# Kernel tuning notes

Measured on AMD Instinct MI355X. Metric: run time of the kernel, lower is better.

## Reference

```python
import jax, jax.numpy as jnp
import numpy as np

D_MODEL = 1024
N_HEADS = 16
MAX_LAG = 512
D_K = D_MODEL // N_HEADS


def setup_inputs() -> dict:
    key = jax.random.key(0)
    ks = jax.random.split(key, 11)
    B, S = 2, 2048
    x = jax.random.normal(ks[0], (B, S, D_MODEL), dtype=jnp.float32)
    lag = jax.random.randint(ks[1], (S,), 0, MAX_LAG + 1, dtype=jnp.int64)
    scale = 1.0 / np.sqrt(D_MODEL)
    wq = jax.random.normal(ks[2], (D_MODEL, D_MODEL), dtype=jnp.float32) * scale
    bq = jnp.zeros((D_MODEL,), dtype=jnp.float32)
    wk = jax.random.normal(ks[3], (D_MODEL, D_MODEL), dtype=jnp.float32) * scale
    bk = jnp.zeros((D_MODEL,), dtype=jnp.float32)
    wv = jax.random.normal(ks[4], (D_MODEL, D_MODEL), dtype=jnp.float32) * scale
    bv = jnp.zeros((D_MODEL,), dtype=jnp.float32)
    wo = jax.random.normal(ks[5], (D_MODEL, D_MODEL), dtype=jnp.float32) * scale
    bo = jnp.zeros((D_MODEL,), dtype=jnp.float32)
    lag_bias = jax.random.normal(ks[6], (N_HEADS, MAX_LAG + 1), dtype=jnp.float32) * 0.02
    return {"x": x, "lag": lag, "wq": wq, "bq": bq, "wk": wk, "bk": bk,
            "wv": wv, "bv": bv, "wo": wo, "bo": bo, "lag_bias": lag_bias}


def reference(x, lag, wq, bq, wk, bk, wv, bv, wo, bo, lag_bias):
    B, S, D = x.shape
    H, dk = N_HEADS, D_K
    # projections: torch Linear is x @ W.T + b; here weights stored as (in, out)
    q = (x @ wq + bq).reshape(B, S, H, dk).transpose(0, 2, 1, 3)  # (B,H,S,dk)
    k = (x @ wk + bk).reshape(B, S, H, dk).transpose(0, 2, 1, 3)
    v = (x @ wv + bv).reshape(B, S, H, dk).transpose(0, 2, 1, 3)
    scores = jnp.einsum('bhqd,bhkd->bhqk', q, k) / jnp.sqrt(jnp.float32(dk))
    ld = jnp.abs(lag[:, None] - lag[None, :]).astype(jnp.int32)  # (S,S)
    bias = lag_bias[:, ld]  # (H,S,S)
    attn = jax.nn.softmax(scores + bias[None], axis=-1)
    out = jnp.einsum('bhqk,bhkd->bhqd', attn, v)
    out = out.transpose(0, 2, 1, 3).reshape(B, S, D)
    return out @ wo + bo
```

## Files before the change

### kernel.cpp

```cpp
#include <hip/hip_runtime.h>

typedef __bf16 bf16;
typedef __bf16 bf16x8 __attribute__((ext_vector_type(8)));
typedef float f32x4 __attribute__((ext_vector_type(4)));

__device__ __forceinline__ f32x4 mfma16(bf16x8 a, bf16x8 b, f32x4 c) {
  return __builtin_amdgcn_mfma_f32_16x16x32_bf16(a, b, c, 0, 0, 0);
}
__device__ __forceinline__ void gload16(const bf16* g, bf16* l) {
  __builtin_amdgcn_global_load_lds((const __attribute__((address_space(1))) unsigned int*)g,
                                   (__attribute__((address_space(3))) unsigned int*)l, 16, 0, 0);
}

__global__ __launch_bounds__(256) void prep_kernel(
    const float* __restrict__ x, const float* __restrict__ wq,
    const float* __restrict__ wk, const float* __restrict__ wv,
    const float* __restrict__ wo, const float* __restrict__ bq,
    const float* __restrict__ bk, const float* __restrict__ bv,
    bf16* __restrict__ xb, bf16* __restrict__ wqkvt, bf16* __restrict__ wot,
    float* __restrict__ bqkv) {
  int blk = blockIdx.x;
  int tid = threadIdx.x;
  if (blk < 2048) {
    int i = blk * 256 + tid;
    const float4* p = (const float4*)x + (size_t)i * 2;
    float4 f0 = p[0], f1 = p[1];
    bf16x8 o;
    o[0] = (bf16)f0.x; o[1] = (bf16)f0.y; o[2] = (bf16)f0.z; o[3] = (bf16)f0.w;
    o[4] = (bf16)f1.x; o[5] = (bf16)f1.y; o[6] = (bf16)f1.z; o[7] = (bf16)f1.w;
    *((bf16x8*)xb + i) = o;
    return;
  }
  if (blk >= 3072) {
    int i = (blk - 3072) * 256 + tid;
    if (i < 1024) bqkv[i] = bq[i];
    else if (i < 2048) bqkv[i] = bk[i - 1024];
    else if (i < 3072) bqkv[i] = bv[i - 2048];
    return;
  }
  __shared__ float t[64][68];
  int sub = blk - 2048;
  int wsel = sub >> 8;
  sub &= 255;
  const float* in = wsel == 0 ? wq : wsel == 1 ? wk : wsel == 2 ? wv : wo;
  bf16* out = (wsel == 3) ? wot : (wqkvt + (size_t)wsel * (1u << 20));
  int bx = sub & 15;
  int by = sub >> 4;
  int r = tid >> 2, p = tid & 3;
  const float* src = in + (size_t)(by * 64 + r) * 1024 + bx * 64 + p * 16;
#pragma unroll
  for (int j = 0; j < 16; j += 4)
    *(float4*)&t[r][p * 16 + j] = *(const float4*)(src + j);
  __syncthreads();
  int n = tid >> 2, sp = tid & 3;
  bf16 tmp[16];
#pragma unroll
  for (int j = 0; j < 16; ++j) tmp[j] = (bf16)t[sp * 16 + j][n];
  bf16* dst = out + (size_t)(bx * 64 + n) * 1024 + by * 64 + sp * 16;
  *(bf16x8*)dst = *(bf16x8*)&tmp[0];
  *(bf16x8*)(dst + 8) = *(bf16x8*)&tmp[8];
}

__global__ __launch_bounds__(256) void sort_lag_kernel(const int* __restrict__ lag,
                                                       int* __restrict__ perm,
                                                       int* __restrict__ slag,
                                                       int* __restrict__ rank) {
  __shared__ int l[2048];
  int tid = threadIdx.x;
  for (int i = tid; i < 2048; i += 256) l[i] = lag[i];
  __syncthreads();
  int i = blockIdx.x * 32 + (tid >> 3);
  int s = tid & 7;
  int vi = l[i];
  int cnt = 0;
  for (int j = s * 256; j < s * 256 + 256; j += 4) {
    int4 vj = *(const int4*)&l[j];
    cnt += (vj.x < vi || (vj.x == vi && (j + 0) < i));
    cnt += (vj.y < vi || (vj.y == vi && (j + 1) < i));
    cnt += (vj.z < vi || (vj.z == vi && (j + 2) < i));
    cnt += (vj.w < vi || (vj.w == vi && (j + 3) < i));
  }
  cnt += __shfl_xor(cnt, 1);
  cnt += __shfl_xor(cnt, 2);
  cnt += __shfl_xor(cnt, 4);
  if (s == 0) { perm[cnt] = i; slag[cnt] = vi; rank[i] = cnt; }
}

__global__ __launch_bounds__(256) void transpose_v_kernel(const bf16* __restrict__ qkv,
                                                          const int* __restrict__ perm,
                                                          bf16* __restrict__ vt) {
  __shared__ bf16 t[64][72];
  int blk = blockIdx.x;
  int st = blk & 31, h = (blk >> 5) & 15, b = blk >> 9;
  int tid = threadIdx.x;
  int r = tid >> 2, p = tid & 3;
  int src_s = perm[st * 64 + r];
  const bf16* src = qkv + (size_t)(b * 2048 + src_s) * 3072 + 2048 + h * 64 + p * 16;
  *(bf16x8*)&t[r][p * 16] = *(const bf16x8*)src;
  *(bf16x8*)&t[r][p * 16 + 8] = *(const bf16x8*)(src + 8);
  __syncthreads();
  int d = tid >> 2, sp = tid & 3;
  bf16 tmp[16];
#pragma unroll
  for (int j = 0; j < 16; ++j) tmp[j] = t[sp * 16 + j][d];
  bf16* dst = vt + (size_t)((b * 16 + h) * 64 + d) * 2048 + st * 64 + sp * 16;
  *(bf16x8*)dst = *(bf16x8*)&tmp[0];
  *(bf16x8*)(dst + 8) = *(bf16x8*)&tmp[8];
}

template <int OUT_BF16, int KFUSE>
__global__ __launch_bounds__(256) void gemm_bt_kernel(
    const bf16* __restrict__ A, const bf16* __restrict__ Bt,
    const float* __restrict__ bias, void* __restrict__ C,
    int M, int N, int K, int scale_cols, float scale_val,
    const int* __restrict__ rank, bf16* __restrict__ kp) {
  __shared__ __align__(16) bf16 As[128 * 64];
  __shared__ __align__(16) bf16 Bs[128 * 64];
  int bn = blockIdx.x * 128, bm = blockIdx.y * 128;
  int tid = threadIdx.x;
  int l = tid & 63;
  int w = tid >> 6;
  int wr = w >> 1, wc = w & 1;
  int g = l >> 4, c = l & 15;
  int swz = (c & 7) << 3;
  int srow = l >> 3;
  int scol = ((l & 7) ^ srow) << 3;
  const bf16* Ap = A + (size_t)(bm + w * 32 + srow) * K + scol;
  const bf16* Bp = Bt + (size_t)(bn + w * 32 + srow) * K + scol;
  bf16* AsW = As + w * 32 * 64;
  bf16* BsW = Bs + w * 32 * 64;

  f32x4 acc[4][4] = {};
  for (int k0 = 0; k0 < K; k0 += 64) {
    __syncthreads();
#pragma unroll
    for (int i = 0; i < 4; ++i) {
      gload16(Ap + (size_t)(8 * i) * K + k0, AsW + i * 512);
      gload16(Bp + (size_t)(8 * i) * K + k0, BsW + i * 512);
    }
    __syncthreads();
#pragma unroll
    for (int kh = 0; kh < 2; ++kh) {
      bf16x8 af[4], bfr[4];
#pragma unroll
      for (int m = 0; m < 4; ++m)
        af[m] = *(const bf16x8*)&As[(wr * 64 + m * 16 + c) * 64 + ((kh * 32 + g * 8) ^ swz)];
#pragma unroll
      for (int n = 0; n < 4; ++n)
        bfr[n] = *(const bf16x8*)&Bs[(wc * 64 + n * 16 + c) * 64 + ((kh * 32 + g * 8) ^ swz)];
#pragma unroll
      for (int m = 0; m < 4; ++m)
#pragma unroll
        for (int n = 0; n < 4; ++n)
          acc[m][n] = mfma16(af[m], bfr[n], acc[m][n]);
    }
  }
  int rowb = bm + wr * 64;
  int colb = bn + wc * 64;
#pragma unroll
  for (int n = 0; n < 4; ++n) {
    int col = colb + n * 16 + c;
    float bv = bias[col];
    float s = (col < scale_cols) ? scale_val : 1.0f;
    bool isk = KFUSE && (col >= 1024) && (col < 2048);
    int hh = (col >> 6) & 15;
    int dd = col & 63;
#pragma unroll
    for (int m = 0; m < 4; ++m) {
      int row = rowb + m * 16 + g * 4;
#pragma unroll
      for (int j = 0; j < 4; ++j) {
        float v = (acc[m][n][j] + bv) * s;
        if (OUT_BF16) {
          if (isk) {
            int rr = row + j;
            int ss = rank[rr & 2047];
            kp[((size_t)((rr >> 11) * 16 + hh) * 2048 + ss) * 64 + dd] = (bf16)v;
          } else {
            ((bf16*)C)[(size_t)(row + j) * N + col] = (bf16)v;
          }
        } else {
          ((float*)C)[(size_t)(row + j) * N + col] = v;
        }
      }
    }
  }
}

__global__ __launch_bounds__(256) void gemm64_kernel(
    const bf16* __restrict__ A, const bf16* __restrict__ Bt,
    const float* __restrict__ bias, float* __restrict__ C,
    int M, int N, int K) {
  __shared__ __align__(16) bf16 As[64 * 64];
  __shared__ __align__(16) bf16 Bs[128 * 64];
  int bn = blockIdx.x * 128, bm = blockIdx.y * 64;
  int tid = threadIdx.x;
  int l = tid & 63;
  int w = tid >> 6;
  int g = l >> 4, c = l & 15;
  int swz = (c & 7) << 3;
  int srow = l >> 3;
  int scol = ((l & 7) ^ srow) << 3;
  const bf16* Ap = A + (size_t)(bm + w * 16 + srow) * K + scol;
  const bf16* Bp = Bt + (size_t)(bn + w * 32 + srow) * K + scol;
  bf16* AsW = As + w * 16 * 64;
  bf16* BsW = Bs + w * 32 * 64;

  f32x4 acc[4][2] = {};
  for (int k0 = 0; k0 < K; k0 += 64) {
    __syncthreads();
#pragma unroll
    for (int i = 0; i < 2; ++i)
      gload16(Ap + (size_t)(8 * i) * K + k0, AsW + i * 512);
#pragma unroll
    for (int i = 0; i < 4; ++i)
      gload16(Bp + (size_t)(8 * i) * K + k0, BsW + i * 512);
    __syncthreads();
#pragma unroll
    for (int kh = 0; kh < 2; ++kh) {
      int koff = (kh * 32 + g * 8) ^ swz;
      bf16x8 af[4], bfr[2];
#pragma unroll
      for (int m = 0; m < 4; ++m)
        af[m] = *(const bf16x8*)&As[(m * 16 + c) * 64 + koff];
#pragma unroll
      for (int n = 0; n < 2; ++n)
        bfr[n] = *(const bf16x8*)&Bs[(w * 32 + n * 16 + c) * 64 + koff];
#pragma unroll
      for (int m = 0; m < 4; ++m)
#pragma unroll
        for (int n = 0; n < 2; ++n)
          acc[m][n] = mfma16(af[m], bfr[n], acc[m][n]);
    }
  }
#pragma unroll
  for (int n = 0; n < 2; ++n) {
    int col = bn + w * 32 + n * 16 + c;
    float bv = bias[col];
#pragma unroll
    for (int m = 0; m < 4; ++m) {
      int row = bm + m * 16 + g * 4;
#pragma unroll
      for (int j = 0; j < 4; ++j)
        C[(size_t)(row + j) * N + col] = acc[m][n][j] + bv;
    }
  }
}

__global__ __launch_bounds__(256) void attn_kernel(
    const bf16* __restrict__ qkv, const bf16* __restrict__ kp,
    const bf16* __restrict__ vt, const int* __restrict__ lag,
    const int* __restrict__ slag, const float* __restrict__ lag_bias,
    bf16* __restrict__ out) {
  __shared__ __align__(16) bf16 Ks0[64 * 64];
  __shared__ __align__(16) bf16 Vs0[64 * 64];
  __shared__ __align__(16) bf16 Ks1[64 * 64];
  __shared__ __align__(16) bf16 Vs1[64 * 64];
  __shared__ __align__(16) bf16 Ps[4][32][72];
  __shared__ float bias2_s[1028];
  __shared__ int lag_s[2048];

  int blk = blockIdx.x;
  blk = (blk & 7) * 64 + (blk >> 3);
  int qt = blk & 15;
  int h = (blk >> 4) & 15;
  int b = blk >> 8;
  int tid = threadIdx.x;
  int w = tid >> 6, l = tid & 63, g = l >> 4, c = l & 15;

  for (int i = tid; i < 1025; i += 256) {
    int d = i - 512;
    d = d < 0 ? -d : d;
    bias2_s[i] = lag_bias[h * 513 + d] * 1.44269504f;
  }
  for (int i = tid; i < 2048; i += 256) lag_s[i] = slag[i];

  int q0 = qt * 128 + w * 32;
  const bf16* qbase = qkv + (size_t)(b * 2048 + q0) * 3072 + h * 64;
  bf16x8 qf[2][2];
#pragma unroll
  for (int m = 0; m < 2; ++m)
#pragma unroll
    for (int kh = 0; kh < 2; ++kh)
      qf[m][kh] = *(const bf16x8*)(qbase + (size_t)(m * 16 + c) * 3072 + kh * 32 + g * 8);

  int lagq[2][4];
#pragma unroll
  for (int m = 0; m < 2; ++m)
#pragma unroll
    for (int j = 0; j < 4; ++j) lagq[m][j] = lag[q0 + m * 16 + g * 4 + j] + 512;

  bf16x8 ones8;
#pragma unroll
  for (int e = 0; e < 8; ++e) ones8[e] = (bf16)1.0f;

  int swz = (c & 7) << 3;
  int off0 = (g * 8) ^ swz;
  int off1 = off0 ^ 32;

  int r0 = w * 16 + (l >> 3);
  int colE = ((l & 7) ^ (l >> 3)) << 3;
  const bf16* kbase = kp + (size_t)(b * 16 + h) * 2048 * 64;
  const bf16* vbase = vt + (size_t)(b * 16 + h) * 64 * 2048;
  const bf16* kg0 = kbase + (size_t)r0 * 64 + colE;
  const bf16* kg1 = kbase + (size_t)(r0 + 8) * 64 + colE;
  const bf16* vg0 = vbase + (size_t)r0 * 2048 + colE;
  const bf16* vg1 = vbase + (size_t)(r0 + 8) * 2048 + colE;

#define STAGE(KD, VD)                    \
  do {                                   \
    gload16(kg0, KD + w * 1024);         \
    gload16(kg1, KD + w * 1024 + 512);   \
    gload16(vg0, VD + w * 1024);         \
    gload16(vg1, VD + w * 1024 + 512);   \
    kg0 += 64 * 64; kg1 += 64 * 64;      \
    vg0 += 64; vg1 += 64;                \
  } while (0)

  STAGE(Ks0, Vs0);
  __syncthreads();

  f32x4 oacc[2][4] = {};
  f32x4 psacc[2] = {};

#define TILE(KB, VB, KT)                                                          \
  do {                                                                            \
    f32x4 sf[2][4] = {};                                                          \
    int lagk[4];                                                                  \
    _Pragma("unroll") for (int kb = 0; kb < 4; ++kb) {                            \
      int row = kb * 16 + c;                                                      \
      bf16x8 k0 = *(const bf16x8*)&KB[row * 64 + off0];                           \
      bf16x8 k1 = *(const bf16x8*)&KB[row * 64 + off1];                           \
      sf[0][kb] = mfma16(qf[0][0], k0, sf[0][kb]);                                \
      sf[0][kb] = mfma16(qf[0][1], k1, sf[0][kb]);                                \
      sf[1][kb] = mfma16(qf[1][0], k0, sf[1][kb]);                                \
      sf[1][kb] = mfma16(qf[1][1], k1, sf[1][kb]);                                \
      lagk[kb] = lag_s[(KT) + kb * 16 + c];                                       \
    }                                                                             \
    _Pragma("unroll") for (int m = 0; m < 2; ++m)                                 \
    _Pragma("unroll") for (int kb = 0; kb < 4; ++kb)                              \
    _Pragma("unroll") for (int j = 0; j < 4; ++j) {                               \
      int ld = lagq[m][j] - lagk[kb];                                             \
      float p = __builtin_amdgcn_exp2f(sf[m][kb][j] + bias2_s[ld]);               \
      Ps[w][m * 16 + g * 4 + j][kb * 16 + c] = (bf16)p;                           \
    }                                                                             \
    asm volatile("s_waitcnt lgkmcnt(0)" ::: "memory");                            \
    _Pragma("unroll") for (int ph = 0; ph < 2; ++ph) {                            \
      bf16x8 pa0 = *(const bf16x8*)&Ps[w][c][ph * 32 + g * 8];                    \
      bf16x8 pa1 = *(const bf16x8*)&Ps[w][16 + c][ph * 32 + g * 8];               \
      int voff = ph ? off1 : off0;                                                \
      _Pragma("unroll") for (int n = 0; n < 4; ++n) {                             \
        bf16x8 vf = *(const bf16x8*)&VB[(n * 16 + c) * 64 + voff];                \
        oacc[0][n] = mfma16(pa0, vf, oacc[0][n]);                                 \
        oacc[1][n] = mfma16(pa1, vf, oacc[1][n]);                                 \
      }                                                                           \
      psacc[0] = mfma16(pa0, ones8, psacc[0]);                                    \
      psacc[1] = mfma16(pa1, ones8, psacc[1]);                                    \
    }                                                                             \
  } while (0)

  for (int kt = 0; kt < 2048; kt += 128) {
    if (kt + 64 < 2048) STAGE(Ks1, Vs1);
    TILE(Ks0, Vs0, kt);
    __syncthreads();
    if (kt + 128 < 2048) STAGE(Ks0, Vs0);
    TILE(Ks1, Vs1, kt + 64);
    __syncthreads();
  }

#pragma unroll
  for (int m = 0; m < 2; ++m) {
#pragma unroll
    for (int j = 0; j < 4; ++j) {
      float inv = 1.f / psacc[m][j];
      bf16* ob = out + (size_t)(b * 2048 + q0 + m * 16 + g * 4 + j) * 1024 + h * 64;
#pragma unroll
      for (int n = 0; n < 4; ++n)
        ob[n * 16 + c] = (bf16)(oacc[m][n][j] * inv);
    }
  }
#undef STAGE
#undef TILE
}

extern "C" void kernel_launch(void* const* d_in, const int* in_sizes, int n_in,
                              void* d_out, int out_size, void* d_ws, size_t ws_size,
                              hipStream_t stream) {
  const float* x        = (const float*)d_in[0];
  const int*   lag      = (const int*)d_in[1];
  const float* wq       = (const float*)d_in[2];
  const float* bq       = (const float*)d_in[3];
  const float* wk       = (const float*)d_in[4];
  const float* bk       = (const float*)d_in[5];
  const float* wv       = (const float*)d_in[6];
  const float* bv       = (const float*)d_in[7];
  const float* wo       = (const float*)d_in[8];
  const float* bo       = (const float*)d_in[9];
  const float* lag_bias = (const float*)d_in[10];

  char* ws = (char*)d_ws;
  bf16*  xb    = (bf16*)ws;
  bf16*  wqkvt = (bf16*)(ws + (8u  << 20));
  bf16*  wot   = (bf16*)(ws + (14u << 20));
  float* bqkv  = (float*)(ws + (16u << 20));
  int*   perm  = (int*)(ws + (16u << 20) + 32768);
  int*   slag  = (int*)(ws + (16u << 20) + 65536);
  int*   rankp = (int*)(ws + (16u << 20) + 98304);
  bf16*  qkv   = (bf16*)(ws + (17u << 20));
  bf16*  vtb   = (bf16*)(ws + (41u << 20));
  bf16*  kpk   = (bf16*)(ws + (49u << 20));
  bf16*  aout  = xb;

  sort_lag_kernel<<<64, 256, 0, stream>>>(lag, perm, slag, rankp);
  prep_kernel<<<3084, 256, 0, stream>>>(x, wq, wk, wv, wo, bq, bk, bv,
                                        xb, wqkvt, wot, bqkv);
  gemm_bt_kernel<1, 1><<<dim3(24, 32), 256, 0, stream>>>(
      xb, wqkvt, bqkv, qkv, 4096, 3072, 1024, 1024, 0.125f * 1.44269504f, rankp, kpk);
  transpose_v_kernel<<<1024, 256, 0, stream>>>(qkv, perm, vtb);
  attn_kernel<<<512, 256, 0, stream>>>(qkv, kpk, vtb, lag, slag, lag_bias, aout);
  gemm64_kernel<<<dim3(8, 64), 256, 0, stream>>>(
      aout, wot, bo, (float*)d_out, 4096, 1024, 1024);
}
```

Measured before the change: 157.8 us.

## Software-pipeline attention QK/softmax against PV and fuse lag sort into prep

Restructures the attention loop so that the QK scores and exponentials for the next key tile are computed while the PV MFMAs for the previous tile consume P from shared memory. V is triple-buffered so staging can run one tile further ahead. Separately, the lag sort kernel is merged into the prep kernel as extra blocks, which removes one launch. The attention change adds LDS use and register pressure from holding the probability registers, and it reorders synchronization.

After: 162.1 us. 2.7% more time.

```diff
diff --git a/kernel.cpp b/kernel.cpp
--- a/kernel.cpp
+++ b/kernel.cpp
@@ -17,8 +17,10 @@
     const float* __restrict__ wk, const float* __restrict__ wv,
     const float* __restrict__ wo, const float* __restrict__ bq,
     const float* __restrict__ bk, const float* __restrict__ bv,
+    const int* __restrict__ lag,
     bf16* __restrict__ xb, bf16* __restrict__ wqkvt, bf16* __restrict__ wot,
-    float* __restrict__ bqkv) {
+    float* __restrict__ bqkv, int* __restrict__ perm, int* __restrict__ slag,
+    int* __restrict__ rank) {
   int blk = blockIdx.x;
   int tid = threadIdx.x;
   if (blk < 2048) {
@@ -31,6 +33,27 @@
     *((bf16x8*)xb + i) = o;
     return;
   }
+  if (blk >= 3084) {
+    __shared__ int l[2048];
+    for (int i = tid; i < 2048; i += 256) l[i] = lag[i];
+    __syncthreads();
+    int i = (blk - 3084) * 32 + (tid >> 3);
+    int s = tid & 7;
+    int vi = l[i];
+    int cnt = 0;
+    for (int j = s * 256; j < s * 256 + 256; j += 4) {
+      int4 vj = *(const int4*)&l[j];
+      cnt += (vj.x < vi || (vj.x == vi && (j + 0) < i));
+      cnt += (vj.y < vi || (vj.y == vi && (j + 1) < i));
+      cnt += (vj.z < vi || (vj.z == vi && (j + 2) < i));
+      cnt += (vj.w < vi || (vj.w == vi && (j + 3) < i));
+    }
+    cnt += __shfl_xor(cnt, 1);
+    cnt += __shfl_xor(cnt, 2);
+    cnt += __shfl_xor(cnt, 4);
+    if (s == 0) { perm[cnt] = i; slag[cnt] = vi; rank[i] = cnt; }
+    return;
+  }
   if (blk >= 3072) {
     int i = (blk - 3072) * 256 + tid;
     if (i < 1024) bqkv[i] = bq[i];
@@ -59,31 +82,6 @@
   bf16* dst = out + (size_t)(bx * 64 + n) * 1024 + by * 64 + sp * 16;
   *(bf16x8*)dst = *(bf16x8*)&tmp[0];
   *(bf16x8*)(dst + 8) = *(bf16x8*)&tmp[8];
-}
-
-__global__ __launch_bounds__(256) void sort_lag_kernel(const int* __restrict__ lag,
-                                                       int* __restrict__ perm,
-                                                       int* __restrict__ slag,
-                                                       int* __restrict__ rank) {
-  __shared__ int l[2048];
-  int tid = threadIdx.x;
-  for (int i = tid; i < 2048; i += 256) l[i] = lag[i];
-  __syncthreads();
-  int i = blockIdx.x * 32 + (tid >> 3);
-  int s = tid & 7;
-  int vi = l[i];
-  int cnt = 0;
-  for (int j = s * 256; j < s * 256 + 256; j += 4) {
-    int4 vj = *(const int4*)&l[j];
-    cnt += (vj.x < vi || (vj.x == vi && (j + 0) < i));
-    cnt += (vj.y < vi || (vj.y == vi && (j + 1) < i));
-    cnt += (vj.z < vi || (vj.z == vi && (j + 2) < i));
-    cnt += (vj.w < vi || (vj.w == vi && (j + 3) < i));
-  }
-  cnt += __shfl_xor(cnt, 1);
-  cnt += __shfl_xor(cnt, 2);
-  cnt += __shfl_xor(cnt, 4);
-  if (s == 0) { perm[cnt] = i; slag[cnt] = vi; rank[i] = cnt; }
 }
 
 __global__ __launch_bounds__(256) void transpose_v_kernel(const bf16* __restrict__ qkv,
@@ -253,9 +251,10 @@
     const int* __restrict__ slag, const float* __restrict__ lag_bias,
     bf16* __restrict__ out) {
   __shared__ __align__(16) bf16 Ks0[64 * 64];
+  __shared__ __align__(16) bf16 Ks1[64 * 64];
   __shared__ __align__(16) bf16 Vs0[64 * 64];
-  __shared__ __align__(16) bf16 Ks1[64 * 64];
   __shared__ __align__(16) bf16 Vs1[64 * 64];
+  __shared__ __align__(16) bf16 Vs2[64 * 64];
   __shared__ __align__(16) bf16 Ps[4][32][72];
   __shared__ float bias2_s[1028];
   __shared__ int lag_s[2048];
@@ -317,40 +316,47 @@
     vg0 += 64; vg1 += 64;                \
   } while (0)
 
-  STAGE(Ks0, Vs0);
-  __syncthreads();
-
   f32x4 oacc[2][4] = {};
   f32x4 psacc[2] = {};
 
-#define TILE(KB, VB, KT)                                                          \
+#define QKSM(KC, T1, PRR)                                                         \
   do {                                                                            \
     f32x4 sf[2][4] = {};                                                          \
     int lagk[4];                                                                  \
     _Pragma("unroll") for (int kb = 0; kb < 4; ++kb) {                            \
       int row = kb * 16 + c;                                                      \
-      bf16x8 k0 = *(const bf16x8*)&KB[row * 64 + off0];                           \
-      bf16x8 k1 = *(const bf16x8*)&KB[row * 64 + off1];                           \
+      bf16x8 k0 = *(const bf16x8*)&KC[row * 64 + off0];                           \
+      bf16x8 k1 = *(const bf16x8*)&KC[row * 64 + off1];                           \
       sf[0][kb] = mfma16(qf[0][0], k0, sf[0][kb]);                                \
       sf[0][kb] = mfma16(qf[0][1], k1, sf[0][kb]);                                \
       sf[1][kb] = mfma16(qf[1][0], k0, sf[1][kb]);                                \
       sf[1][kb] = mfma16(qf[1][1], k1, sf[1][kb]);                                \
-      lagk[kb] = lag_s[(KT) + kb * 16 + c];                                       \
+      lagk[kb] = lag_s[(T1) * 64 + kb * 16 + c];                                  \
     }                                                                             \
     _Pragma("unroll") for (int m = 0; m < 2; ++m)                                 \
     _Pragma("unroll") for (int kb = 0; kb < 4; ++kb)                              \
     _Pragma("unroll") for (int j = 0; j < 4; ++j) {                               \
       int ld = lagq[m][j] - lagk[kb];                                             \
-      float p = __builtin_amdgcn_exp2f(sf[m][kb][j] + bias2_s[ld]);               \
-      Ps[w][m * 16 + g * 4 + j][kb * 16 + c] = (bf16)p;                           \
+      PRR[m][kb * 4 + j] = __builtin_amdgcn_exp2f(sf[m][kb][j] + bias2_s[ld]);    \
     }                                                                             \
-    asm volatile("s_waitcnt lgkmcnt(0)" ::: "memory");                            \
+  } while (0)
+
+#define PSWRITE(PRR)                                                              \
+  do {                                                                            \
+    _Pragma("unroll") for (int m = 0; m < 2; ++m)                                 \
+    _Pragma("unroll") for (int kb = 0; kb < 4; ++kb)                              \
+    _Pragma("unroll") for (int j = 0; j < 4; ++j)                                 \
+      Ps[w][m * 16 + g * 4 + j][kb * 16 + c] = (bf16)PRR[m][kb * 4 + j];          \
+  } while (0)
+
+#define PVSTEP(VR)                                                                \
+  do {                                                                            \
     _Pragma("unroll") for (int ph = 0; ph < 2; ++ph) {                            \
       bf16x8 pa0 = *(const bf16x8*)&Ps[w][c][ph * 32 + g * 8];                    \
       bf16x8 pa1 = *(const bf16x8*)&Ps[w][16 + c][ph * 32 + g * 8];               \
       int voff = ph ? off1 : off0;                                                \
       _Pragma("unroll") for (int n = 0; n < 4; ++n) {                             \
-        bf16x8 vf = *(const bf16x8*)&VB[(n * 16 + c) * 64 + voff];                \
+        bf16x8 vf = *(const bf16x8*)&VR[(n * 16 + c) * 64 + voff];                \
         oacc[0][n] = mfma16(pa0, vf, oacc[0][n]);                                 \
         oacc[1][n] = mfma16(pa1, vf, oacc[1][n]);                                 \
       }                                                                           \
@@ -359,14 +365,36 @@
     }                                                                             \
   } while (0)
 
-  for (int kt = 0; kt < 2048; kt += 128) {
-    if (kt + 64 < 2048) STAGE(Ks1, Vs1);
-    TILE(Ks0, Vs0, kt);
-    __syncthreads();
-    if (kt + 128 < 2048) STAGE(Ks0, Vs0);
-    TILE(Ks1, Vs1, kt + 64);
-    __syncthreads();
-  }
+#define BODYX(KC, KS, VR, VS, T1, DOSTAGE)                                        \
+  do {                                                                            \
+    __syncthreads();                                                              \
+    if (DOSTAGE) { STAGE(KS, VS); }                                               \
+    float pr[2][16];                                                              \
+    QKSM(KC, T1, pr);                                                             \
+    PVSTEP(VR);                                                                   \
+    PSWRITE(pr);                                                                  \
+  } while (0)
+
+  STAGE(Ks0, Vs0);
+  __syncthreads();
+  STAGE(Ks1, Vs1);
+  {
+    float pr[2][16];
+    QKSM(Ks0, 0, pr);
+    PSWRITE(pr);
+  }
+
+  for (int tb = 0; tb < 30; tb += 6) {
+    BODYX(Ks1, Ks0, Vs0, Vs2, tb + 1, 1);
+    BODYX(Ks0, Ks1, Vs1, Vs0, tb + 2, 1);
+    BODYX(Ks1, Ks0, Vs2, Vs1, tb + 3, 1);
+    BODYX(Ks0, Ks1, Vs0, Vs2, tb + 4, 1);
+    BODYX(Ks1, Ks0, Vs1, Vs0, tb + 5, 1);
+    BODYX(Ks0, Ks1, Vs2, Vs1, tb + 6, 1);
+  }
+  BODYX(Ks1, Ks0, Vs0, Vs2, 31, 0);
+  asm volatile("s_waitcnt lgkmcnt(0)" ::: "memory");
+  PVSTEP(Vs1);
 
 #pragma unroll
   for (int m = 0; m < 2; ++m) {
@@ -380,7 +408,10 @@
     }
   }
 #undef STAGE
-#undef TILE
+#undef QKSM
+#undef PSWRITE
+#undef PVSTEP
+#undef BODYX
 }
 
 extern "C" void kernel_launch(void* const* d_in, const int* in_sizes, int n_in,
@@ -411,9 +442,8 @@
   bf16*  kpk   = (bf16*)(ws + (49u << 20));
   bf16*  aout  = xb;
 
-  sort_lag_kernel<<<64, 256, 0, stream>>>(lag, perm, slag, rankp);
-  prep_kernel<<<3084, 256, 0, stream>>>(x, wq, wk, wv, wo, bq, bk, bv,
-                                        xb, wqkvt, wot, bqkv);
+  prep_kernel<<<3148, 256, 0, stream>>>(x, wq, wk, wv, wo, bq, bk, bv, lag,
+                                        xb, wqkvt, wot, bqkv, perm, slag, rankp);
   gemm_bt_kernel<1, 1><<<dim3(24, 32), 256, 0, stream>>>(
       xb, wqkvt, bqkv, qkv, 4096, 3072, 1024, 1024, 0.125f * 1.44269504f, rankp, kpk);
   transpose_v_kernel<<<1024, 256, 0, stream>>>(qkv, perm, vtb);
```
